# Kernel optimization log

Measured on AMD Instinct MI355X. Metric: run time of the kernel, lower is better.

## Reference

```python
import jax, jax.numpy as jnp
import numpy as np

# Multi-scale feature pyramid (H, W) per level, as produced by a DETR backbone
SPATIAL_SHAPES = [(100, 100), (50, 50), (25, 25), (13, 13)]
LEVEL_START = np.cumsum([0] + [h * w for h, w in SPATIAL_SHAPES])[:-1]
LEN = sum(h * w for h, w in SPATIAL_SHAPES)  # 13294
B = 2
D = 256      # d_model
NH = 8       # n_heads
NL = 4       # n_levels
NP = 4       # n_points
DH = D // NH
DFF = 1024
EPS = 1e-5


def setup_inputs() -> dict:
    key = jax.random.key(0)
    ks = jax.random.split(key, 16)
    w = lambda k, sh: jax.random.normal(k, sh, jnp.float32) * 0.02
    return {
        'src': jax.random.normal(ks[0], (B, LEN, D), jnp.float32),
        'pos': jax.random.normal(ks[1], (B, LEN, D), jnp.float32) * 0.02,
        'reference_points': jax.random.uniform(ks[2], (B, LEN, NL, 2), jnp.float32),
        'W_value': w(ks[3], (D, D)), 'b_value': jnp.zeros((D,), jnp.float32),
        'W_off': w(ks[4], (D, NH * NL * NP * 2)), 'b_off': w(ks[5], (NH * NL * NP * 2,)),
        'W_attn': w(ks[6], (D, NH * NL * NP)), 'b_attn': jnp.zeros((NH * NL * NP,), jnp.float32),
        'W_out': w(ks[7], (D, D)), 'b_out': jnp.zeros((D,), jnp.float32),
        'W1': w(ks[8], (D, DFF)), 'b1': jnp.zeros((DFF,), jnp.float32),
        'W2': w(ks[9], (DFF, D)), 'b2': jnp.zeros((D,), jnp.float32),
        'g1': jnp.ones((D,), jnp.float32), 'be1': jnp.zeros((D,), jnp.float32),
        'g2': jnp.ones((D,), jnp.float32), 'be2': jnp.zeros((D,), jnp.float32),
    }


def layer_norm(x, g, b):
    m = jnp.mean(x, -1, keepdims=True)
    v = jnp.mean((x - m) ** 2, -1, keepdims=True)
    return (x - m) * jax.lax.rsqrt(v + EPS) * g + b


def ms_deform_attn(query, src, ref, W_value, b_value, W_off, b_off, W_attn, b_attn, W_out, b_out):
    Bq, L, _ = query.shape
    value = (src @ W_value + b_value).reshape(Bq, L, NH, DH)
    off = (query @ W_off + b_off).reshape(Bq, L, NH, NL, NP, 2)
    attw = jax.nn.softmax((query @ W_attn + b_attn).reshape(Bq, L, NH, NL * NP), axis=-1)
    attw = attw.reshape(Bq, L, NH, NL, NP)
    # normalizer is (W, H) per level, matching offset_normalizer in MSDeformAttn
    wh = jnp.array([[w_, h_] for h_, w_ in SPATIAL_SHAPES], jnp.float32)
    loc = ref[:, :, None, :, None, :] + off / wh[None, None, None, :, None, :]  # (B,L,NH,NL,NP,2)

    out = jnp.zeros((Bq, L, NH, DH), value.dtype)
    for l, (H, W) in enumerate(SPATIAL_SHAPES):
        s = int(LEVEL_START[l])
        vl = value[:, s:s + H * W]  # (B, H*W, NH, DH)
        # grid_sample(align_corners=False): pixel = loc * size - 0.5
        x = loc[:, :, :, l, :, 0] * W - 0.5  # (B, L, NH, NP)
        y = loc[:, :, :, l, :, 1] * H - 0.5
        x = jnp.transpose(x, (0, 1, 3, 2)).reshape(Bq, L * NP, NH)
        y = jnp.transpose(y, (0, 1, 3, 2)).reshape(Bq, L * NP, NH)
        x0 = jnp.floor(x); y0 = jnp.floor(y)
        dx = x - x0; dy = y - y0
        x0i = x0.astype(jnp.int32); y0i = y0.astype(jnp.int32)
        acc = jnp.zeros((Bq, L * NP, NH, DH), value.dtype)
        corners = [
            (x0i,     y0i,     (1 - dx) * (1 - dy)),
            (x0i + 1, y0i,     dx * (1 - dy)),
            (x0i,     y0i + 1, (1 - dx) * dy),
            (x0i + 1, y0i + 1, dx * dy),
        ]
        for xi, yi, wgt in corners:
            inb = (xi >= 0) & (xi < W) & (yi >= 0) & (yi < H)  # zero padding
            idx = jnp.clip(yi, 0, H - 1) * W + jnp.clip(xi, 0, W - 1)
            g = jnp.take_along_axis(vl, idx[..., None], axis=1)  # (B, L*NP, NH, DH)
            acc = acc + g * (wgt * inb)[..., None]
        acc = acc.reshape(Bq, L, NP, NH, DH)
        w_l = jnp.transpose(attw[:, :, :, l, :], (0, 1, 3, 2))  # (B, L, NP, NH)
        out = out + jnp.sum(acc * w_l[..., None], axis=2)
    return out.reshape(Bq, L, D) @ W_out + b_out


def reference(src, pos, reference_points,
              W_value, b_value, W_off, b_off, W_attn, b_attn, W_out, b_out,
              W1, b1, W2, b2, g1, be1, g2, be2):
    # DeformableTransformerEncoderLayer.forward (dropout = identity at eval)
    query = src + pos
    src2 = ms_deform_attn(query, src, reference_points,
                          W_value, b_value, W_off, b_off, W_attn, b_attn, W_out, b_out)
    src = layer_norm(src + src2, g1, be1)
    ffn = jax.nn.relu(src @ W1 + b1) @ W2 + b2
    src = layer_norm(src + ffn, g2, be2)
    return src
```

## Files before the change

kernel.cpp:

```cpp
#include <hip/hip_runtime.h>
#include <hip/hip_bf16.h>

#define LENQ 13294
#define MROWS 26588
#define PADM  26624
#define EPS_LN 1e-5f

typedef __attribute__((ext_vector_type(8))) short short8;
typedef __attribute__((ext_vector_type(4))) float vf4;

__device__ inline ushort f2bf(float f) {
    __hip_bfloat16 h = __float2bfloat16(f);
    return reinterpret_cast<ushort&>(h);
}
__device__ inline float bfbits2f(uint lo16) {
    return __uint_as_float(lo16 << 16);
}
__device__ inline float lo16f(uint u) { return __uint_as_float(u << 16); }
__device__ inline float hi16f(uint u) { return __uint_as_float(u & 0xffff0000u); }

__device__ inline void load_lds16(const void* g, void* l) {
    __builtin_amdgcn_global_load_lds(
        (const __attribute__((address_space(1))) unsigned int*)g,
        (__attribute__((address_space(3))) unsigned int*)l,
        16, 0, 0);
}

__global__ __launch_bounds__(256) void wconv_all(
    const float* __restrict__ Wv, const float* __restrict__ Woff,
    const float* __restrict__ Wattn, const float* __restrict__ Wout,
    const float* __restrict__ W1, const float* __restrict__ W2,
    ushort* __restrict__ wvt, ushort* __restrict__ woat,
    ushort* __restrict__ woutt, ushort* __restrict__ w1t, ushort* __restrict__ w2t)
{
    const int bid = blockIdx.x;
    const float* src; ushort* dst; int K, N, tb;
    if      (bid < 64)  { src = Wv;    dst = wvt;            K = 256;  N = 256;  tb = bid; }
    else if (bid < 128) { src = Woff;  dst = woat;           K = 256;  N = 256;  tb = bid - 64; }
    else if (bid < 160) { src = Wattn; dst = woat + 256*256; K = 256;  N = 128;  tb = bid - 128; }
    else if (bid < 224) { src = Wout;  dst = woutt;          K = 256;  N = 256;  tb = bid - 160; }
    else if (bid < 480) { src = W1;    dst = w1t;            K = 256;  N = 1024; tb = bid - 224; }
    else                { src = W2;    dst = w2t;            K = 1024; N = 256;  tb = bid - 480; }
    const int ntn = N >> 5;
    const int kt = tb / ntn, nt = tb % ntn;

    __shared__ float s[32][36];
    const int t = threadIdx.x;
    const int ty = t >> 3, tx = (t & 7) * 4;
    float4 v = *reinterpret_cast<const float4*>(src + (size_t)(kt*32 + ty) * N + nt*32 + tx);
    s[ty][tx+0] = v.x; s[ty][tx+1] = v.y; s[ty][tx+2] = v.z; s[ty][tx+3] = v.w;
    __syncthreads();
    ushort4 o;
    o.x = f2bf(s[tx+0][ty]); o.y = f2bf(s[tx+1][ty]);
    o.z = f2bf(s[tx+2][ty]); o.w = f2bf(s[tx+3][ty]);
    *reinterpret_cast<ushort4*>(dst + (size_t)(nt*32 + ty) * K + kt*32 + tx) = o;
}

__global__ __launch_bounds__(256) void conv_src_q(
    const float* __restrict__ src, const float* __restrict__ pos,
    ushort* __restrict__ srcb, ushort* __restrict__ qb)
{
    const int i = blockIdx.x * 256 + threadIdx.x;
    const int row = i >> 6;
    const int c4 = i & 63;
    const int sr = min(row, MROWS - 1);
    float4 s = reinterpret_cast<const float4*>(src)[(size_t)sr * 64 + c4];
    float4 p = reinterpret_cast<const float4*>(pos)[(size_t)sr * 64 + c4];
    ushort4 sb, qv;
    sb.x = f2bf(s.x); sb.y = f2bf(s.y); sb.z = f2bf(s.z); sb.w = f2bf(s.w);
    qv.x = f2bf(s.x + p.x); qv.y = f2bf(s.y + p.y);
    qv.z = f2bf(s.z + p.z); qv.w = f2bf(s.w + p.w);
    reinterpret_cast<ushort4*>(srcb)[(size_t)row * 64 + c4] = sb;
    reinterpret_cast<ushort4*>(qb)[(size_t)row * 64 + c4]   = qv;
}

template<int MF, bool RELU>
__global__ __launch_bounds__(256) void gemm_lds(
    const ushort* __restrict__ A, const ushort* __restrict__ Bt,
    const float* __restrict__ bias0, const float* __restrict__ bias1, int nsplit,
    ushort* __restrict__ C, int N, int K)
{
    constexpr int BM = MF * 32;
    __shared__ short As[2][BM * 32];
    __shared__ short Bs[2][128 * 32];

    const int t = threadIdx.x;
    const int m0 = blockIdx.x * BM, n0 = blockIdx.y * 128;
    const int lane = t & 63, w = t >> 6;
    const int wr = w >> 1, wc = w & 1;
    const int ln = lane & 15, lr = lane >> 4;
    const int swz = (lr ^ ((ln >> 1) & 3)) * 8;
    const int cg = (((lane & 3) ^ ((lane >> 3) & 3))) * 8;
    const int srow = lane >> 2;

    vf4 acc[MF][4];
    #pragma unroll
    for (int m = 0; m < MF; ++m)
        #pragma unroll
        for (int n = 0; n < 4; ++n)
            acc[m][n] = (vf4){0.f, 0.f, 0.f, 0.f};

    const int ach0 = (MF == 4) ? 2 * w : w;
    const ushort* gA0 = A + (size_t)(m0 + ach0 * 16 + srow) * K + cg;
    const ushort* gA1 = A + (size_t)(m0 + (2 * w + 1) * 16 + srow) * K + cg;
    const ushort* gB0 = Bt + (size_t)(n0 + (2 * w) * 16 + srow) * K + cg;
    const ushort* gB1 = Bt + (size_t)(n0 + (2 * w + 1) * 16 + srow) * K + cg;
    const int lA0 = ach0 * 512, lA1 = (2 * w + 1) * 512;
    const int lB0 = (2 * w) * 512, lB1 = (2 * w + 1) * 512;

#define STAGE_TILE(buf, kk) do {                                        \
        load_lds16(gA0 + (kk), &As[buf][lA0]);                          \
        if constexpr (MF == 4) load_lds16(gA1 + (kk), &As[buf][lA1]);   \
        load_lds16(gB0 + (kk), &Bs[buf][lB0]);                          \
        load_lds16(gB1 + (kk), &Bs[buf][lB1]);                          \
    } while (0)

    STAGE_TILE(0, 0);
    int cur = 0;
    for (int k0 = 0; k0 < K; k0 += 32) {
        __syncthreads();
        if (k0 + 32 < K) STAGE_TILE(cur ^ 1, k0 + 32);

        short8 af[MF], bfr[4];
        #pragma unroll
        for (int m = 0; m < MF; ++m)
            af[m] = *reinterpret_cast<const short8*>(
                &As[cur][(wr * (MF * 16) + m * 16 + ln) * 32 + swz]);
        #pragma unroll
        for (int n = 0; n < 4; ++n)
            bfr[n] = *reinterpret_cast<const short8*>(
                &Bs[cur][(wc * 64 + n * 16 + ln) * 32 + swz]);
        #pragma unroll
        for (int m = 0; m < MF; ++m)
            #pragma unroll
            for (int n = 0; n < 4; ++n)
                acc[m][n] = __builtin_amdgcn_mfma_f32_16x16x32_bf16(af[m], bfr[n], acc[m][n], 0, 0, 0);
        cur ^= 1;
    }
#undef STAGE_TILE

    #pragma unroll
    for (int n = 0; n < 4; ++n) {
        const int col = n0 + wc * 64 + n * 16 + ln;
        const float b = (col < nsplit) ? bias0[col] : bias1[col - nsplit];
        #pragma unroll
        for (int m = 0; m < MF; ++m) {
            const int rbase = m0 + wr * (MF * 16) + m * 16 + lr * 4;
            #pragma unroll
            for (int q = 0; q < 4; ++q) {
                float v = acc[m][n][q] + b;
                if (RELU) v = fmaxf(v, 0.f);
                C[(size_t)(rbase + q) * N + col] = f2bf(v);
            }
        }
    }
}

__global__ __launch_bounds__(256) void ms_sample(
    const ushort* __restrict__ value, const ushort* __restrict__ oa,
    const float* __restrict__ ref, ushort* __restrict__ outb)
{
    __shared__ uint2 s_iw[64 * 66];

    const int t    = threadIdx.x;
    const int row0 = blockIdx.x * 8;

    #pragma unroll
    for (int j = 0; j < 4; ++j) {
        const int item = t + j * 256;
        const int r = item >> 7, h = (item >> 4) & 7, lp = item & 15;
        const int l = lp >> 2;
        const int row = min(row0 + r, MROWS - 1);
        const int bsel = (row >= LENQ) ? 1 : 0;

        const float lg = bfbits2f(oa[(size_t)row * 384 + 256 + h * 16 + lp]);
        float mx = lg;
        #pragma unroll
        for (int s2 = 1; s2 < 16; s2 <<= 1) mx = fmaxf(mx, __shfl_xor(mx, s2));
        const float e = __expf(lg - mx);
        float se = e;
        #pragma unroll
        for (int s2 = 1; s2 < 16; s2 <<= 1) se += __shfl_xor(se, s2);
        const float aw = e / se;

        const int W = (int)((0x0D193264u >> (l * 8)) & 0xffu);
        const int LS = (l == 0) ? 0 : (l == 1) ? 10000 : (l == 2) ? 12500 : 13125;
        const uint oxy = *reinterpret_cast<const uint*>(oa + (size_t)row * 384 + (h * 16 + lp) * 2);
        const float ox = lo16f(oxy);
        const float oy = hi16f(oxy);
        const float rx = ref[(size_t)row * 8 + l * 2 + 0];
        const float ry = ref[(size_t)row * 8 + l * 2 + 1];
        const float fw = (float)W;
        const float x = (rx + ox / fw) * fw - 0.5f;
        const float y = (ry + oy / fw) * fw - 0.5f;
        const float fx = floorf(x), fy = floorf(y);
        const float dx = x - fx, dy = y - fy;
        const int x0 = (int)fx, y0 = (int)fy;
        const int x1i = x0 + 1, y1i = y0 + 1;
        const int gbase = bsel * LENQ + LS;

        const bool inx0 = (x0 >= 0) && (x0 < W), inx1 = (x1i >= 0) && (x1i < W);
        const bool iny0 = (y0 >= 0) && (y0 < W), iny1 = (y1i >= 0) && (y1i < W);
        const int xc0 = min(max(x0, 0), W - 1), xc1 = min(max(x1i, 0), W - 1);
        const int yc0 = min(max(y0, 0), W - 1), yc1 = min(max(y1i, 0), W - 1);
        const float w00 = (inx0 && iny0) ? (1.f - dx) * (1.f - dy) * aw : 0.f;
        const float w10 = (inx1 && iny0) ? dx * (1.f - dy) * aw : 0.f;
        const float w01 = (inx0 && iny1) ? (1.f - dx) * dy * aw : 0.f;
        const float w11 = (inx1 && iny1) ? dx * dy * aw : 0.f;
        const uint b0 = (uint)(gbase + yc0 * W);
        const uint b1 = (uint)(gbase + yc1 * W);
        uint4 c01, c23;
        c01.x = (b0 + (uint)xc0) * 512u; c01.y = __float_as_uint(w00);
        c01.z = (b0 + (uint)xc1) * 512u; c01.w = __float_as_uint(w10);
        c23.x = (b1 + (uint)xc0) * 512u; c23.y = __float_as_uint(w01);
        c23.z = (b1 + (uint)xc1) * 512u; c23.w = __float_as_uint(w11);
        uint4* dst = reinterpret_cast<uint4*>(&s_iw[(r * 8 + h) * 66 + lp * 4]);
        dst[0] = c01;
        dst[1] = c23;
    }
    __syncthreads();

    const int g = t >> 2, cq = t & 3;
    const int r = g >> 3, h = g & 7;
    const char* vbase = (const char*)value + h * 64 + cq * 16;
    const uint4* iw = reinterpret_cast<const uint4*>(&s_iw[g * 66]);
    float acc[8] = {0.f, 0.f, 0.f, 0.f, 0.f, 0.f, 0.f, 0.f};
    #pragma unroll 4
    for (int e2 = 0; e2 < 32; ++e2) {
        const uint4 p = iw[e2];
        {
            const uint4 gv = *reinterpret_cast<const uint4*>(vbase + p.x);
            const float w0 = __uint_as_float(p.y);
            acc[0] += w0 * lo16f(gv.x); acc[1] += w0 * hi16f(gv.x);
            acc[2] += w0 * lo16f(gv.y); acc[3] += w0 * hi16f(gv.y);
            acc[4] += w0 * lo16f(gv.z); acc[5] += w0 * hi16f(gv.z);
            acc[6] += w0 * lo16f(gv.w); acc[7] += w0 * hi16f(gv.w);
        }
        {
            const uint4 gv = *reinterpret_cast<const uint4*>(vbase + p.z);
            const float w1 = __uint_as_float(p.w);
            acc[0] += w1 * lo16f(gv.x); acc[1] += w1 * hi16f(gv.x);
            acc[2] += w1 * lo16f(gv.y); acc[3] += w1 * hi16f(gv.y);
            acc[4] += w1 * lo16f(gv.z); acc[5] += w1 * hi16f(gv.z);
            acc[6] += w1 * lo16f(gv.w); acc[7] += w1 * hi16f(gv.w);
        }
    }
    const int row = row0 + r;
    if (row < MROWS) {
        uint4 o;
        o.x = (uint)f2bf(acc[0]) | ((uint)f2bf(acc[1]) << 16);
        o.y = (uint)f2bf(acc[2]) | ((uint)f2bf(acc[3]) << 16);
        o.z = (uint)f2bf(acc[4]) | ((uint)f2bf(acc[5]) << 16);
        o.w = (uint)f2bf(acc[6]) | ((uint)f2bf(acc[7]) << 16);
        *reinterpret_cast<uint4*>((char*)outb + (size_t)row * 512 + h * 64 + cq * 16) = o;
    }
}

template<bool AF32, bool WF32>
__global__ __launch_bounds__(256) void resid_ln(
    const float* __restrict__ af, const ushort* __restrict__ ab,
    const ushort* __restrict__ r,
    const float* __restrict__ g, const float* __restrict__ be,
    float* __restrict__ outf, ushort* __restrict__ outb, int M)
{
    const int lane = threadIdx.x & 63;
    const int wid  = threadIdx.x >> 6;
    const int row  = blockIdx.x * 4 + wid;
    if (row >= M) return;

    float4 va;
    if (AF32) {
        va = *(reinterpret_cast<const float4*>(af + (size_t)row * 256) + lane);
    } else {
        ushort4 ua = *(reinterpret_cast<const ushort4*>(ab + (size_t)row * 256) + lane);
        va.x = bfbits2f(ua.x); va.y = bfbits2f(ua.y);
        va.z = bfbits2f(ua.z); va.w = bfbits2f(ua.w);
    }
    ushort4 ur = *(reinterpret_cast<const ushort4*>(r + (size_t)row * 256) + lane);
    float4 v;
    v.x = va.x + bfbits2f(ur.x); v.y = va.y + bfbits2f(ur.y);
    v.z = va.z + bfbits2f(ur.z); v.w = va.w + bfbits2f(ur.w);

    float s = v.x + v.y + v.z + v.w;
    #pragma unroll
    for (int m = 1; m < 64; m <<= 1) s += __shfl_xor(s, m);
    const float mean = s * (1.f / 256.f);

    float4 d;
    d.x = v.x - mean; d.y = v.y - mean; d.z = v.z - mean; d.w = v.w - mean;
    float q = d.x * d.x + d.y * d.y + d.z * d.z + d.w * d.w;
    #pragma unroll
    for (int m = 1; m < 64; m <<= 1) q += __shfl_xor(q, m);
    const float rs = rsqrtf(q * (1.f / 256.f) + EPS_LN);

    float4 gv = *(reinterpret_cast<const float4*>(g) + lane);
    float4 bv = *(reinterpret_cast<const float4*>(be) + lane);
    float4 o;
    o.x = d.x * rs * gv.x + bv.x;
    o.y = d.y * rs * gv.y + bv.y;
    o.z = d.z * rs * gv.z + bv.z;
    o.w = d.w * rs * gv.w + bv.w;
    if (WF32) {
        *(reinterpret_cast<float4*>(outf + (size_t)row * 256) + lane) = o;
    } else {
        ushort4 h;
        h.x = f2bf(o.x); h.y = f2bf(o.y); h.z = f2bf(o.z); h.w = f2bf(o.w);
        *(reinterpret_cast<ushort4*>(outb + (size_t)row * 256) + lane) = h;
    }
}

extern "C" void kernel_launch(void* const* d_in, const int* in_sizes, int n_in,
                              void* d_out, int out_size, void* d_ws, size_t ws_size,
                              hipStream_t stream)
{
    const float* src   = (const float*)d_in[0];
    const float* pos   = (const float*)d_in[1];
    const float* refp  = (const float*)d_in[2];
    const float* Wv    = (const float*)d_in[3];
    const float* bv    = (const float*)d_in[4];
    const float* Woff  = (const float*)d_in[5];
    const float* boff  = (const float*)d_in[6];
    const float* Wattn = (const float*)d_in[7];
    const float* battn = (const float*)d_in[8];
    const float* Wout  = (const float*)d_in[9];
    const float* bout  = (const float*)d_in[10];
    const float* W1    = (const float*)d_in[11];
    const float* b1    = (const float*)d_in[12];
    const float* W2    = (const float*)d_in[13];
    const float* b2    = (const float*)d_in[14];
    const float* g1    = (const float*)d_in[15];
    const float* be1   = (const float*)d_in[16];
    const float* g2    = (const float*)d_in[17];
    const float* be2   = (const float*)d_in[18];
    float* out = (float*)d_out;

    char* wsb = (char*)d_ws;
    const size_t SB   = (size_t)PADM * 256 * 2;
    const size_t OABS = (size_t)PADM * 384 * 2;
    ushort* srcb   = (ushort*)(wsb);
    ushort* qb     = (ushort*)(wsb + SB);
    ushort* valueb = (ushort*)(wsb + 2 * SB);
    ushort* oab    = (ushort*)(wsb + 3 * SB);
    ushort* attnb  = (ushort*)(wsb + 3 * SB + OABS);
    ushort* src2b  = (ushort*)(wsb + 4 * SB + OABS);
    ushort* ffnb   = src2b;
    ushort* x1b    = (ushort*)(wsb + 5 * SB + OABS);
    ushort* hb     = (ushort*)(wsb);
    char*   wgt    = wsb + 6 * SB + OABS;
    ushort* wvt    = (ushort*)(wgt);
    ushort* woat   = (ushort*)(wgt + 131072);
    ushort* woutt  = (ushort*)(wgt + 327680);
    ushort* w1t    = (ushort*)(wgt + 458752);
    ushort* w2t    = (ushort*)(wgt + 983040);

    const dim3 blk(256);

    wconv_all<<<dim3(736), blk, 0, stream>>>(Wv, Woff, Wattn, Wout, W1, W2,
                                             wvt, woat, woutt, w1t, w2t);

    conv_src_q<<<dim3(PADM / 4), blk, 0, stream>>>(src, pos, srcb, qb);

    gemm_lds<2, false><<<dim3(416, 2), blk, 0, stream>>>(
        srcb, wvt, bv, bv, 256, valueb, 256, 256);

    gemm_lds<2, false><<<dim3(416, 3), blk, 0, stream>>>(
        qb, woat, boff, battn, 256, oab, 384, 256);

    ms_sample<<<dim3(3324), blk, 0, stream>>>(valueb, oab, refp, attnb);

    gemm_lds<2, false><<<dim3(416, 2), blk, 0, stream>>>(
        attnb, woutt, bout, bout, 256, src2b, 256, 256);

    resid_ln<true, false><<<dim3(6647), blk, 0, stream>>>(
        src, nullptr, src2b, g1, be1, nullptr, x1b, MROWS);

    gemm_lds<4, true><<<dim3(208, 8), blk, 0, stream>>>(
        x1b, w1t, b1, b1, 1024, hb, 1024, 256);

    gemm_lds<2, false><<<dim3(416, 2), blk, 0, stream>>>(
        hb, w2t, b2, b2, 256, ffnb, 256, 1024);

    resid_ln<false, true><<<dim3(6647), blk, 0, stream>>>(
        nullptr, x1b, ffnb, g2, be2, out, nullptr, MROWS);
}
```

Before: 182.4 us.

## Merge prep and projection launches, pack bilinear weights as bf16 with dot2

Weight transposition and the src/query conversion now run in one launch, and the value and offset/attention projection GEMMs share a single grid. Fewer launches cut launch overhead and tail gaps. The sampling kernel now stores the four corner offsets and bf16-packed bilinear weights per point in separate LDS arrays. It accumulates with fdot2 bf16 instructions, pairing corners via byte permutes, to cut LDS footprint and ALU work. Rounding the bilinear weights to bf16 costs some accuracy.

Result: faster. 172.5 us (-5.5%).

```diff
diff --git a/kernel.cpp b/kernel.cpp
--- a/kernel.cpp
+++ b/kernel.cpp
@@ -8,16 +8,24 @@
 
 typedef __attribute__((ext_vector_type(8))) short short8;
 typedef __attribute__((ext_vector_type(4))) float vf4;
+typedef __attribute__((ext_vector_type(2))) __bf16 bf16x2;
 
 __device__ inline ushort f2bf(float f) {
     __hip_bfloat16 h = __float2bfloat16(f);
     return reinterpret_cast<ushort&>(h);
 }
-__device__ inline float bfbits2f(uint lo16) {
-    return __uint_as_float(lo16 << 16);
-}
+__device__ inline float bfbits2f(uint lo16) { return __uint_as_float(lo16 << 16); }
 __device__ inline float lo16f(uint u) { return __uint_as_float(u << 16); }
 __device__ inline float hi16f(uint u) { return __uint_as_float(u & 0xffff0000u); }
+
+#if __has_builtin(__builtin_amdgcn_fdot2_f32_bf16) && __has_builtin(__builtin_amdgcn_perm)
+#define USE_DOT2 1
+__device__ inline bf16x2 u2bf2(uint u) { return __builtin_bit_cast(bf16x2, u); }
+#define SEL_EVEN 0x01000504u
+#define SEL_ODD  0x03020706u
+#else
+#define USE_DOT2 0
+#endif
 
 __device__ inline void load_lds16(const void* g, void* l) {
     __builtin_amdgcn_global_load_lds(
@@ -26,66 +34,61 @@
         16, 0, 0);
 }
 
-__global__ __launch_bounds__(256) void wconv_all(
+__global__ __launch_bounds__(256) void prep_all(
     const float* __restrict__ Wv, const float* __restrict__ Woff,
     const float* __restrict__ Wattn, const float* __restrict__ Wout,
     const float* __restrict__ W1, const float* __restrict__ W2,
     ushort* __restrict__ wvt, ushort* __restrict__ woat,
-    ushort* __restrict__ woutt, ushort* __restrict__ w1t, ushort* __restrict__ w2t)
-{
+    ushort* __restrict__ woutt, ushort* __restrict__ w1t, ushort* __restrict__ w2t,
+    const float* __restrict__ srcf, const float* __restrict__ posf,
+    ushort* __restrict__ srcb, ushort* __restrict__ qb)
+{
+    __shared__ float s[32][36];
     const int bid = blockIdx.x;
-    const float* src; ushort* dst; int K, N, tb;
-    if      (bid < 64)  { src = Wv;    dst = wvt;            K = 256;  N = 256;  tb = bid; }
-    else if (bid < 128) { src = Woff;  dst = woat;           K = 256;  N = 256;  tb = bid - 64; }
-    else if (bid < 160) { src = Wattn; dst = woat + 256*256; K = 256;  N = 128;  tb = bid - 128; }
-    else if (bid < 224) { src = Wout;  dst = woutt;          K = 256;  N = 256;  tb = bid - 160; }
-    else if (bid < 480) { src = W1;    dst = w1t;            K = 256;  N = 1024; tb = bid - 224; }
-    else                { src = W2;    dst = w2t;            K = 1024; N = 256;  tb = bid - 480; }
-    const int ntn = N >> 5;
-    const int kt = tb / ntn, nt = tb % ntn;
-
-    __shared__ float s[32][36];
     const int t = threadIdx.x;
-    const int ty = t >> 3, tx = (t & 7) * 4;
-    float4 v = *reinterpret_cast<const float4*>(src + (size_t)(kt*32 + ty) * N + nt*32 + tx);
-    s[ty][tx+0] = v.x; s[ty][tx+1] = v.y; s[ty][tx+2] = v.z; s[ty][tx+3] = v.w;
-    __syncthreads();
-    ushort4 o;
-    o.x = f2bf(s[tx+0][ty]); o.y = f2bf(s[tx+1][ty]);
-    o.z = f2bf(s[tx+2][ty]); o.w = f2bf(s[tx+3][ty]);
-    *reinterpret_cast<ushort4*>(dst + (size_t)(nt*32 + ty) * K + kt*32 + tx) = o;
-}
-
-__global__ __launch_bounds__(256) void conv_src_q(
-    const float* __restrict__ src, const float* __restrict__ pos,
-    ushort* __restrict__ srcb, ushort* __restrict__ qb)
-{
-    const int i = blockIdx.x * 256 + threadIdx.x;
-    const int row = i >> 6;
-    const int c4 = i & 63;
-    const int sr = min(row, MROWS - 1);
-    float4 s = reinterpret_cast<const float4*>(src)[(size_t)sr * 64 + c4];
-    float4 p = reinterpret_cast<const float4*>(pos)[(size_t)sr * 64 + c4];
-    ushort4 sb, qv;
-    sb.x = f2bf(s.x); sb.y = f2bf(s.y); sb.z = f2bf(s.z); sb.w = f2bf(s.w);
-    qv.x = f2bf(s.x + p.x); qv.y = f2bf(s.y + p.y);
-    qv.z = f2bf(s.z + p.z); qv.w = f2bf(s.w + p.w);
-    reinterpret_cast<ushort4*>(srcb)[(size_t)row * 64 + c4] = sb;
-    reinterpret_cast<ushort4*>(qb)[(size_t)row * 64 + c4]   = qv;
+    if (bid < 736) {
+        const float* src; ushort* dst; int K, N, tb;
+        if      (bid < 64)  { src = Wv;    dst = wvt;            K = 256;  N = 256;  tb = bid; }
+        else if (bid < 128) { src = Woff;  dst = woat;           K = 256;  N = 256;  tb = bid - 64; }
+        else if (bid < 160) { src = Wattn; dst = woat + 256*256; K = 256;  N = 128;  tb = bid - 128; }
+        else if (bid < 224) { src = Wout;  dst = woutt;          K = 256;  N = 256;  tb = bid - 160; }
+        else if (bid < 480) { src = W1;    dst = w1t;            K = 256;  N = 1024; tb = bid - 224; }
+        else                { src = W2;    dst = w2t;            K = 1024; N = 256;  tb = bid - 480; }
+        const int ntn = N >> 5;
+        const int kt = tb / ntn, nt = tb % ntn;
+        const int ty = t >> 3, tx = (t & 7) * 4;
+        float4 v = *reinterpret_cast<const float4*>(src + (size_t)(kt*32 + ty) * N + nt*32 + tx);
+        s[ty][tx+0] = v.x; s[ty][tx+1] = v.y; s[ty][tx+2] = v.z; s[ty][tx+3] = v.w;
+        __syncthreads();
+        ushort4 o;
+        o.x = f2bf(s[tx+0][ty]); o.y = f2bf(s[tx+1][ty]);
+        o.z = f2bf(s[tx+2][ty]); o.w = f2bf(s[tx+3][ty]);
+        *reinterpret_cast<ushort4*>(dst + (size_t)(nt*32 + ty) * K + kt*32 + tx) = o;
+    } else {
+        const int i = (bid - 736) * 256 + t;
+        const int row = i >> 6;
+        const int c4 = i & 63;
+        const int sr = min(row, MROWS - 1);
+        float4 sv = reinterpret_cast<const float4*>(srcf)[(size_t)sr * 64 + c4];
+        float4 pv = reinterpret_cast<const float4*>(posf)[(size_t)sr * 64 + c4];
+        ushort4 sb, qv;
+        sb.x = f2bf(sv.x); sb.y = f2bf(sv.y); sb.z = f2bf(sv.z); sb.w = f2bf(sv.w);
+        qv.x = f2bf(sv.x + pv.x); qv.y = f2bf(sv.y + pv.y);
+        qv.z = f2bf(sv.z + pv.z); qv.w = f2bf(sv.w + pv.w);
+        reinterpret_cast<ushort4*>(srcb)[(size_t)row * 64 + c4] = sb;
+        reinterpret_cast<ushort4*>(qb)[(size_t)row * 64 + c4]   = qv;
+    }
 }
 
 template<int MF, bool RELU>
-__global__ __launch_bounds__(256) void gemm_lds(
+__device__ __forceinline__ void gemm_body(
     const ushort* __restrict__ A, const ushort* __restrict__ Bt,
     const float* __restrict__ bias0, const float* __restrict__ bias1, int nsplit,
-    ushort* __restrict__ C, int N, int K)
+    ushort* __restrict__ C, int N, int K, int m0, int n0,
+    short* AsP, short* BsP)
 {
     constexpr int BM = MF * 32;
-    __shared__ short As[2][BM * 32];
-    __shared__ short Bs[2][128 * 32];
-
     const int t = threadIdx.x;
-    const int m0 = blockIdx.x * BM, n0 = blockIdx.y * 128;
     const int lane = t & 63, w = t >> 6;
     const int wr = w >> 1, wc = w & 1;
     const int ln = lane & 15, lr = lane >> 4;
@@ -108,11 +111,11 @@
     const int lA0 = ach0 * 512, lA1 = (2 * w + 1) * 512;
     const int lB0 = (2 * w) * 512, lB1 = (2 * w + 1) * 512;
 
-#define STAGE_TILE(buf, kk) do {                                        \
-        load_lds16(gA0 + (kk), &As[buf][lA0]);                          \
-        if constexpr (MF == 4) load_lds16(gA1 + (kk), &As[buf][lA1]);   \
-        load_lds16(gB0 + (kk), &Bs[buf][lB0]);                          \
-        load_lds16(gB1 + (kk), &Bs[buf][lB1]);                          \
+#define STAGE_TILE(buf, kk) do {                                              \
+        load_lds16(gA0 + (kk), AsP + (buf) * (BM * 32) + lA0);                \
+        if constexpr (MF == 4) load_lds16(gA1 + (kk), AsP + (buf) * (BM * 32) + lA1); \
+        load_lds16(gB0 + (kk), BsP + (buf) * (128 * 32) + lB0);               \
+        load_lds16(gB1 + (kk), BsP + (buf) * (128 * 32) + lB1);               \
     } while (0)
 
     STAGE_TILE(0, 0);
@@ -125,11 +128,11 @@
         #pragma unroll
         for (int m = 0; m < MF; ++m)
             af[m] = *reinterpret_cast<const short8*>(
-                &As[cur][(wr * (MF * 16) + m * 16 + ln) * 32 + swz]);
+                AsP + cur * (BM * 32) + (wr * (MF * 16) + m * 16 + ln) * 32 + swz);
         #pragma unroll
         for (int n = 0; n < 4; ++n)
             bfr[n] = *reinterpret_cast<const short8*>(
-                &Bs[cur][(wc * 64 + n * 16 + ln) * 32 + swz]);
+                BsP + cur * (128 * 32) + (wc * 64 + n * 16 + ln) * 32 + swz);
         #pragma unroll
         for (int m = 0; m < MF; ++m)
             #pragma unroll
@@ -156,11 +159,44 @@
     }
 }
 
+template<int MF, bool RELU>
+__global__ __launch_bounds__(256) void gemm_single(
+    const ushort* __restrict__ A, const ushort* __restrict__ Bt,
+    const float* __restrict__ bias0, const float* __restrict__ bias1, int nsplit,
+    ushort* __restrict__ C, int N, int K)
+{
+    constexpr int BM = MF * 32;
+    __shared__ short As[2 * BM * 32];
+    __shared__ short Bs[2 * 128 * 32];
+    gemm_body<MF, RELU>(A, Bt, bias0, bias1, nsplit, C, N, K,
+                        blockIdx.x * BM, blockIdx.y * 128, As, Bs);
+}
+
+__global__ __launch_bounds__(256) void gemm_pair(
+    const ushort* __restrict__ srcb, const ushort* __restrict__ wvt,
+    const float* __restrict__ bv, ushort* __restrict__ valueb,
+    const ushort* __restrict__ qb, const ushort* __restrict__ woat,
+    const float* __restrict__ boff, const float* __restrict__ battn,
+    ushort* __restrict__ oab)
+{
+    __shared__ short As[2 * 64 * 32];
+    __shared__ short Bs[2 * 128 * 32];
+    const int by = blockIdx.y;
+    if (by < 2) {
+        gemm_body<2, false>(srcb, wvt, bv, bv, 256, valueb, 256, 256,
+                            blockIdx.x * 64, by * 128, As, Bs);
+    } else {
+        gemm_body<2, false>(qb, woat, boff, battn, 256, oab, 384, 256,
+                            blockIdx.x * 64, (by - 2) * 128, As, Bs);
+    }
+}
+
 __global__ __launch_bounds__(256) void ms_sample(
     const ushort* __restrict__ value, const ushort* __restrict__ oa,
     const float* __restrict__ ref, ushort* __restrict__ outb)
 {
-    __shared__ uint2 s_iw[64 * 66];
+    __shared__ uint s_off[64 * 68];
+    __shared__ uint s_w[64 * 34];
 
     const int t    = threadIdx.x;
     const int row0 = blockIdx.x * 8;
@@ -209,43 +245,52 @@
         const float w11 = (inx1 && iny1) ? dx * dy * aw : 0.f;
         const uint b0 = (uint)(gbase + yc0 * W);
         const uint b1 = (uint)(gbase + yc1 * W);
-        uint4 c01, c23;
-        c01.x = (b0 + (uint)xc0) * 512u; c01.y = __float_as_uint(w00);
-        c01.z = (b0 + (uint)xc1) * 512u; c01.w = __float_as_uint(w10);
-        c23.x = (b1 + (uint)xc0) * 512u; c23.y = __float_as_uint(w01);
-        c23.z = (b1 + (uint)xc1) * 512u; c23.w = __float_as_uint(w11);
-        uint4* dst = reinterpret_cast<uint4*>(&s_iw[(r * 8 + h) * 66 + lp * 4]);
-        dst[0] = c01;
-        dst[1] = c23;
+        const int g = r * 8 + h;
+        *reinterpret_cast<uint4*>(&s_off[g * 68 + lp * 4]) =
+            make_uint4((b0 + (uint)xc0) * 512u, (b0 + (uint)xc1) * 512u,
+                       (b1 + (uint)xc0) * 512u, (b1 + (uint)xc1) * 512u);
+        const uint wA = (uint)f2bf(w00) | ((uint)f2bf(w10) << 16);
+        const uint wB = (uint)f2bf(w01) | ((uint)f2bf(w11) << 16);
+        *reinterpret_cast<uint2*>(&s_w[g * 34 + lp * 2]) = make_uint2(wA, wB);
     }
     __syncthreads();
 
     const int g = t >> 2, cq = t & 3;
-    const int r = g >> 3, h = g & 7;
+    const int h = g & 7;
     const char* vbase = (const char*)value + h * 64 + cq * 16;
-    const uint4* iw = reinterpret_cast<const uint4*>(&s_iw[g * 66]);
     float acc[8] = {0.f, 0.f, 0.f, 0.f, 0.f, 0.f, 0.f, 0.f};
-    #pragma unroll 4
-    for (int e2 = 0; e2 < 32; ++e2) {
-        const uint4 p = iw[e2];
-        {
-            const uint4 gv = *reinterpret_cast<const uint4*>(vbase + p.x);
-            const float w0 = __uint_as_float(p.y);
-            acc[0] += w0 * lo16f(gv.x); acc[1] += w0 * hi16f(gv.x);
-            acc[2] += w0 * lo16f(gv.y); acc[3] += w0 * hi16f(gv.y);
-            acc[4] += w0 * lo16f(gv.z); acc[5] += w0 * hi16f(gv.z);
-            acc[6] += w0 * lo16f(gv.w); acc[7] += w0 * hi16f(gv.w);
-        }
-        {
-            const uint4 gv = *reinterpret_cast<const uint4*>(vbase + p.z);
-            const float w1 = __uint_as_float(p.w);
-            acc[0] += w1 * lo16f(gv.x); acc[1] += w1 * hi16f(gv.x);
-            acc[2] += w1 * lo16f(gv.y); acc[3] += w1 * hi16f(gv.y);
-            acc[4] += w1 * lo16f(gv.z); acc[5] += w1 * hi16f(gv.z);
-            acc[6] += w1 * lo16f(gv.w); acc[7] += w1 * hi16f(gv.w);
-        }
-    }
-    const int row = row0 + r;
+    #pragma unroll 2
+    for (int pt = 0; pt < 16; ++pt) {
+        const uint4 o4 = *reinterpret_cast<const uint4*>(&s_off[g * 68 + pt * 4]);
+        const uint2 wp = *reinterpret_cast<const uint2*>(&s_w[g * 34 + pt * 2]);
+        const uint4 g00 = *reinterpret_cast<const uint4*>(vbase + o4.x);
+        const uint4 g10 = *reinterpret_cast<const uint4*>(vbase + o4.y);
+        const uint4 g01 = *reinterpret_cast<const uint4*>(vbase + o4.z);
+        const uint4 g11 = *reinterpret_cast<const uint4*>(vbase + o4.w);
+#if USE_DOT2
+#define CORNER2(u0, u1, wpk, klo, khi)                                                 \
+        acc[klo] = __builtin_amdgcn_fdot2_f32_bf16(                                    \
+            u2bf2(__builtin_amdgcn_perm((u0), (u1), SEL_EVEN)), u2bf2(wpk), acc[klo], false); \
+        acc[khi] = __builtin_amdgcn_fdot2_f32_bf16(                                    \
+            u2bf2(__builtin_amdgcn_perm((u0), (u1), SEL_ODD)),  u2bf2(wpk), acc[khi], false);
+        CORNER2(g00.x, g10.x, wp.x, 0, 1) CORNER2(g01.x, g11.x, wp.y, 0, 1)
+        CORNER2(g00.y, g10.y, wp.x, 2, 3) CORNER2(g01.y, g11.y, wp.y, 2, 3)
+        CORNER2(g00.z, g10.z, wp.x, 4, 5) CORNER2(g01.z, g11.z, wp.y, 4, 5)
+        CORNER2(g00.w, g10.w, wp.x, 6, 7) CORNER2(g01.w, g11.w, wp.y, 6, 7)
+#undef CORNER2
+#else
+        const float w00f = lo16f(wp.x), w10f = hi16f(wp.x);
+        const float w01f = lo16f(wp.y), w11f = hi16f(wp.y);
+#define CORNER1(gv, wf)                                                   \
+        acc[0] += (wf) * lo16f(gv.x); acc[1] += (wf) * hi16f(gv.x);       \
+        acc[2] += (wf) * lo16f(gv.y); acc[3] += (wf) * hi16f(gv.y);       \
+        acc[4] += (wf) * lo16f(gv.z); acc[5] += (wf) * hi16f(gv.z);       \
+        acc[6] += (wf) * lo16f(gv.w); acc[7] += (wf) * hi16f(gv.w);
+        CORNER1(g00, w00f) CORNER1(g10, w10f) CORNER1(g01, w01f) CORNER1(g11, w11f)
+#undef CORNER1
+#endif
+    }
+    const int row = row0 + (g >> 3);
     if (row < MROWS) {
         uint4 o;
         o.x = (uint)f2bf(acc[0]) | ((uint)f2bf(acc[1]) << 16);
@@ -355,29 +400,25 @@
 
     const dim3 blk(256);
 
-    wconv_all<<<dim3(736), blk, 0, stream>>>(Wv, Woff, Wattn, Wout, W1, W2,
-                                             wvt, woat, woutt, w1t, w2t);
-
-    conv_src_q<<<dim3(PADM / 4), blk, 0, stream>>>(src, pos, srcb, qb);
-
-    gemm_lds<2, false><<<dim3(416, 2), blk, 0, stream>>>(
-        srcb, wvt, bv, bv, 256, valueb, 256, 256);
-
-    gemm_lds<2, false><<<dim3(416, 3), blk, 0, stream>>>(
-        qb, woat, boff, battn, 256, oab, 384, 256);
+    prep_all<<<dim3(736 + PADM / 4), blk, 0, stream>>>(
+        Wv, Woff, Wattn, Wout, W1, W2, wvt, woat, woutt, w1t, w2t,
+        src, pos, srcb, qb);
+
+    gemm_pair<<<dim3(416, 5), blk, 0, stream>>>(
+        srcb, wvt, bv, valueb, qb, woat, boff, battn, oab);
 
     ms_sample<<<dim3(3324), blk, 0, stream>>>(valueb, oab, refp, attnb);
 
-    gemm_lds<2, false><<<dim3(416, 2), blk, 0, stream>>>(
+    gemm_single<2, false><<<dim3(416, 2), blk, 0, stream>>>(
         attnb, woutt, bout, bout, 256, src2b, 256, 256);
 
     resid_ln<true, false><<<dim3(6647), blk, 0, stream>>>(
         src, nullptr, src2b, g1, be1, nullptr, x1b, MROWS);
 
-    gemm_lds<4, true><<<dim3(208, 8), blk, 0, stream>>>(
+    gemm_single<4, true><<<dim3(208, 8), blk, 0, stream>>>(
         x1b, w1t, b1, b1, 1024, hb, 1024, 256);
 
-    gemm_lds<2, false><<<dim3(416, 2), blk, 0, stream>>>(
+    gemm_single<2, false><<<dim3(416, 2), blk, 0, stream>>>(
         hb, w2t, b2, b2, 256, ffnb, 256, 1024);
 
     resid_ln<false, true><<<dim3(6647), blk, 0, stream>>>(
```
